# Kernel optimization log

Measured on AMD Instinct MI355X. Metric: run time of the kernel, lower is better.

Reference implementation:

```python
import jax, jax.numpy as jnp
import numpy as np

DIM = 1024
NUM_HEADS = 16
HEAD_DIM = DIM // NUM_HEADS
HIDDEN = 4 * DIM
EPS = 1e-5


def rmsnorm(x, w):
    var = jnp.mean(jnp.square(x), axis=-1, keepdims=True)
    return x * jax.lax.rsqrt(var + EPS) * w


def setup_inputs() -> dict:
    key = jax.random.key(0)
    ks = jax.random.split(key, 10)
    s = 0.02
    return {
        "x": jax.random.normal(ks[0], (2, 2048, DIM), dtype=jnp.float32),
        "wq": jax.random.normal(ks[1], (DIM, DIM), dtype=jnp.float32) * s,
        "wk": jax.random.normal(ks[2], (DIM, DIM), dtype=jnp.float32) * s,
        "wv": jax.random.normal(ks[3], (DIM, DIM), dtype=jnp.float32) * s,
        "wo": jax.random.normal(ks[4], (DIM, DIM), dtype=jnp.float32) * s,
        "wgate": jax.random.normal(ks[5], (HIDDEN, DIM), dtype=jnp.float32) * s,
        "wup": jax.random.normal(ks[6], (HIDDEN, DIM), dtype=jnp.float32) * s,
        "wdown": jax.random.normal(ks[7], (DIM, HIDDEN), dtype=jnp.float32) * s,
        "norm1_w": jnp.ones((DIM,), dtype=jnp.float32),
        "norm2_w": jnp.ones((DIM,), dtype=jnp.float32),
    }


def reference(x, wq, wk, wv, wo, wgate, wup, wdown, norm1_w, norm2_w):
    B, S, _ = x.shape
    residual = x
    h = rmsnorm(x, norm1_w)
    # torch Linear: y = x @ W.T  (W is [out, in])
    q = (h @ wq.T).reshape(B, S, NUM_HEADS, HEAD_DIM)
    k = (h @ wk.T).reshape(B, S, NUM_HEADS, HEAD_DIM)
    v = (h @ wv.T).reshape(B, S, NUM_HEADS, HEAD_DIM)
    scale = HEAD_DIM ** -0.5
    # [B, H, S, S] scores, causal mask
    scores = jnp.einsum("bqhd,bkhd->bhqk", q, k) * scale
    causal = jnp.tril(jnp.ones((S, S), dtype=bool))
    scores = jnp.where(causal, scores, -jnp.inf)
    attn = jax.nn.softmax(scores, axis=-1)
    out = jnp.einsum("bhqk,bkhd->bqhd", attn, v).reshape(B, S, DIM)
    x = residual + out @ wo.T
    residual = x
    h = rmsnorm(x, norm2_w)
    mlp = (jax.nn.silu(h @ wgate.T) * (h @ wup.T)) @ wdown.T
    return residual + mlp
```

## Files before the change

kernel.cpp:

```cpp
#include <hip/hip_runtime.h>
#include <stdint.h>

typedef __attribute__((ext_vector_type(4))) float  f32x4;
typedef __attribute__((ext_vector_type(8))) __bf16 bf16x8;
typedef __attribute__((ext_vector_type(4))) unsigned short us4;

__device__ __forceinline__ unsigned short f2bf(float f) {
  unsigned int u = __float_as_uint(f);
  unsigned int r = (u + 0x7fffu + ((u >> 16) & 1u)) >> 16;
  return (unsigned short)r;
}
__device__ __forceinline__ float bf2f(unsigned short h) {
  return __uint_as_float(((unsigned int)h) << 16);
}
__device__ __forceinline__ void gload16(const void* g, void* l) {
  __builtin_amdgcn_global_load_lds((const __attribute__((address_space(1))) void*)g,
                                   (__attribute__((address_space(3))) void*)l, 16, 0, 0);
}

__global__ __launch_bounds__(256) void convert_w(
    const float* __restrict__ wq, const float* __restrict__ wk, const float* __restrict__ wv,
    const float* __restrict__ wo, const float* __restrict__ wg, const float* __restrict__ wu,
    const float* __restrict__ wd, unsigned short* __restrict__ dst)
{
  long vid = (long)blockIdx.x * 256 + threadIdx.x;
  long e = vid * 4;
  const float* s; long base;
  if (e < (1L << 22)) { int wi = (int)(e >> 20); s = wi == 0 ? wq : wi == 1 ? wk : wi == 2 ? wv : wo; base = (long)wi << 20; }
  else if (e < (2L << 22)) { s = wg; base = 1L << 22; }
  else if (e < (3L << 22)) { s = wu; base = 2L << 22; }
  else                     { s = wd; base = 3L << 22; }
  f32x4 v = *(const f32x4*)(s + (e - base));
  us4 o; o.x = f2bf(v.x); o.y = f2bf(v.y); o.z = f2bf(v.z); o.w = f2bf(v.w);
  *(us4*)(dst + e) = o;
}

__global__ __launch_bounds__(256) void rmsnorm_k(const float* __restrict__ x,
                                                 const float* __restrict__ w,
                                                 unsigned short* __restrict__ h)
{
  const int row = blockIdx.x, t = threadIdx.x;
  const float* xr = x + (long)row * 1024;
  f32x4 v = *(const f32x4*)(xr + t * 4);
  float ss = v.x * v.x + v.y * v.y + v.z * v.z + v.w * v.w;
  #pragma unroll
  for (int o = 32; o > 0; o >>= 1) ss += __shfl_xor(ss, o);
  __shared__ float red[4];
  if ((t & 63) == 0) red[t >> 6] = ss;
  __syncthreads();
  ss = red[0] + red[1] + red[2] + red[3];
  float sc = rsqrtf(ss * (1.0f / 1024.0f) + 1e-5f);
  f32x4 wv = *(const f32x4*)(w + t * 4);
  us4 o4;
  o4.x = f2bf(v.x * sc * wv.x);
  o4.y = f2bf(v.y * sc * wv.y);
  o4.z = f2bf(v.z * sc * wv.z);
  o4.w = f2bf(v.w * sc * wv.w);
  *(us4*)(h + (long)row * 1024 + t * 4) = o4;
}

template<int EPI, int BM>
__global__ __launch_bounds__(256) void gemm_bt(
    const unsigned short* __restrict__ A, const unsigned short* __restrict__ B,
    int M, int N, int K, void* __restrict__ out0,
    const float* __restrict__ resid, const unsigned short* __restrict__ gbuf)
{
  constexpr int MI = (BM == 128) ? 4 : 2;
  __shared__ __align__(16) unsigned short Al[BM * 64];
  __shared__ __align__(16) unsigned short Bl[128 * 64];
  const int t = threadIdx.x;
  const int lane = t & 63;
  const int wid = t >> 6;
  const int wr = wid >> 1, wc = wid & 1;
  const long m0 = (long)blockIdx.x * BM;
  const long n0 = (long)blockIdx.y * 128;
  const int lr = lane & 15, lk = (lane >> 4) * 8;
  f32x4 acc[MI][4] = {};
  const int trow = t >> 3, tcol = (t & 7) * 8;
  const unsigned short* Ag = A + (m0 + trow) * (long)K + tcol;
  const unsigned short* Bg = B + (n0 + trow) * (long)K + tcol;
  unsigned short* Ald = Al + trow * 64 + tcol;
  unsigned short* Bld = Bl + trow * 64 + tcol;
  const int nkt = K >> 6;
  for (int kt = 0; kt < nkt; ++kt) {
    #pragma unroll
    for (int i = 0; i < BM / 32; ++i)
      gload16(Ag + (long)kt * 64 + (long)i * 32 * K, Ald + i * 2048);
    #pragma unroll
    for (int i = 0; i < 4; ++i)
      gload16(Bg + (long)kt * 64 + (long)i * 32 * K, Bld + i * 2048);
    __syncthreads();
    #pragma unroll
    for (int kk = 0; kk < 64; kk += 32) {
      bf16x8 af[MI], bfr[4];
      #pragma unroll
      for (int mi = 0; mi < MI; ++mi)
        af[mi] = *(const bf16x8*)&Al[(wr * (MI * 16) + mi * 16 + lr) * 64 + kk + lk];
      #pragma unroll
      for (int ni = 0; ni < 4; ++ni)
        bfr[ni] = *(const bf16x8*)&Bl[(wc * 64 + ni * 16 + lr) * 64 + kk + lk];
      #pragma unroll
      for (int mi = 0; mi < MI; ++mi)
        #pragma unroll
        for (int ni = 0; ni < 4; ++ni)
          acc[mi][ni] = __builtin_amdgcn_mfma_f32_16x16x32_bf16(af[mi], bfr[ni], acc[mi][ni], 0, 0, 0);
    }
    __syncthreads();
  }
  const int lg = lane >> 4;
  #pragma unroll
  for (int mi = 0; mi < MI; ++mi)
    #pragma unroll
    for (int ni = 0; ni < 4; ++ni)
      #pragma unroll
      for (int j = 0; j < 4; ++j) {
        long row = m0 + wr * (MI * 16) + mi * 16 + lg * 4 + j;
        long col = n0 + wc * 64 + ni * 16 + lr;
        float v = acc[mi][ni][j];
        if (EPI == 0) {
          unsigned short* qkv = (unsigned short*)out0;
          long b = row >> 11, s = row & 2047;
          if (col < 1024) {
            long hh = col >> 6, d = col & 63;
            qkv[((b * 16 + hh) * 2048 + s) * 64 + d] = f2bf(v);
          } else if (col < 2048) {
            long c = col - 1024, hh = c >> 6, d = c & 63;
            qkv[4194304 + ((b * 16 + hh) * 2048 + s) * 64 + d] = f2bf(v);
          } else {
            long c = col - 2048, hh = c >> 6, d = c & 63;
            qkv[8388608 + ((b * 16 + hh) * 64 + d) * 2048 + s] = f2bf(v);
          }
        } else if (EPI == 1) {
          ((float*)out0)[row * N + col] = resid[row * N + col] + v;
        } else if (EPI == 2) {
          ((unsigned short*)out0)[row * N + col] = f2bf(v);
        } else {
          float g = bf2f(gbuf[row * N + col]);
          float sg = g / (1.0f + __expf(-g));
          ((unsigned short*)out0)[row * N + col] = f2bf(sg * v);
        }
      }
}

__global__ __launch_bounds__(256) void attn_k(
    const unsigned short* __restrict__ qb, const unsigned short* __restrict__ kb,
    const unsigned short* __restrict__ vtb, unsigned short* __restrict__ ob)
{
  __shared__ __align__(16) unsigned short Kl[2 * 4096];
  __shared__ __align__(16) unsigned short Vl[2 * 4096];
  __shared__ __align__(16) unsigned short Pl[4 * 1024];
  const int t = threadIdx.x, lane = t & 63, w = t >> 6;
  const int pid = blockIdx.x;
  const int bh = blockIdx.y;
  const int lr = lane & 15, lg = lane >> 4;
  const long kvbase = (long)bh * 2048 * 64;
  const float SC = 0.125f * 1.4426950408889634f;

  const int trow = t >> 3;
  const int csw = (((t & 7) ^ (trow & 7)) * 8);
  auto stage = [&](int buf, int kt2) {
    #pragma unroll
    for (int i = 0; i < 2; ++i) {
      gload16(&kb[kvbase + (long)(kt2 * 64 + i * 32 + trow) * 64 + csw],
              &Kl[buf * 4096 + i * 2048 + t * 8]);
      gload16(&vtb[kvbase + (long)(i * 32 + trow) * 2048 + kt2 * 64 + csw],
              &Vl[buf * 4096 + i * 2048 + t * 8]);
    }
  };
  auto swz = [](const unsigned short* base, int row, int col) -> const bf16x8* {
    int b = ((row << 7) + (col << 1)) ^ ((row & 7) << 4);
    return (const bf16x8*)((const char*)base + b);
  };

  #pragma unroll 1
  for (int pass = 0; pass < 2; ++pass) {
    const int qt = pass ? pid : (31 - pid);
    const int q0 = qt * 64;
    bf16x8 qf[2];
    #pragma unroll
    for (int kk = 0; kk < 2; ++kk)
      qf[kk] = *(const bf16x8*)&qb[kvbase + (long)(q0 + w * 16 + lr) * 64 + kk * 32 + lg * 8];
    f32x4 oacc[4] = {};
    float mi_[4], li_[4];
    #pragma unroll
    for (int j = 0; j < 4; ++j) { mi_[j] = -1e30f; li_[j] = 0.f; }

    stage(0, 0);
    __syncthreads();
    int cur = 0;
    for (int kt = 0; kt <= qt; ++kt) {
      if (kt < qt) stage(cur ^ 1, kt + 1);
      f32x4 sa[4] = {};
      #pragma unroll
      for (int kk = 0; kk < 2; ++kk)
        #pragma unroll
        for (int ni = 0; ni < 4; ++ni) {
          bf16x8 kf = *swz(&Kl[cur * 4096], ni * 16 + lr, kk * 32 + lg * 8);
          sa[ni] = __builtin_amdgcn_mfma_f32_16x16x32_bf16(qf[kk], kf, sa[ni], 0, 0, 0);
        }
      float p[4][4];
      const bool diag = (kt == qt);
      #pragma unroll
      for (int ni = 0; ni < 4; ++ni)
        #pragma unroll
        for (int j = 0; j < 4; ++j) {
          float sv = sa[ni][j] * SC;
          if (diag && (ni * 16 + lr > w * 16 + lg * 4 + j)) sv = -1e30f;
          p[ni][j] = sv;
        }
      float mx4[4];
      #pragma unroll
      for (int j = 0; j < 4; ++j) {
        float mx = fmaxf(fmaxf(p[0][j], p[1][j]), fmaxf(p[2][j], p[3][j]));
        mx = fmaxf(mx, __shfl_xor(mx, 1));
        mx = fmaxf(mx, __shfl_xor(mx, 2));
        mx = fmaxf(mx, __shfl_xor(mx, 4));
        mx = fmaxf(mx, __shfl_xor(mx, 8));
        mx4[j] = mx;
      }
      float g = fmaxf(fmaxf(mx4[0] - mi_[0], mx4[1] - mi_[1]),
                      fmaxf(mx4[2] - mi_[2], mx4[3] - mi_[3]));
      if (!__all(g <= 8.0f)) {
        #pragma unroll
        for (int j = 0; j < 4; ++j) {
          float mnew = fmaxf(mi_[j], mx4[j]);
          float a = exp2f(mi_[j] - mnew);
          mi_[j] = mnew;
          li_[j] *= a;
          #pragma unroll
          for (int f = 0; f < 4; ++f) oacc[f][j] *= a;
        }
      }
      #pragma unroll
      for (int j = 0; j < 4; ++j) {
        float rs = 0.f;
        #pragma unroll
        for (int ni = 0; ni < 4; ++ni) { float e = exp2f(p[ni][j] - mi_[j]); p[ni][j] = e; rs += e; }
        rs += __shfl_xor(rs, 1); rs += __shfl_xor(rs, 2);
        rs += __shfl_xor(rs, 4); rs += __shfl_xor(rs, 8);
        li_[j] += rs;
      }
      unsigned short* pw = &Pl[w * 1024];
      #pragma unroll
      for (int ni = 0; ni < 4; ++ni)
        #pragma unroll
        for (int j = 0; j < 4; ++j) {
          int row = lg * 4 + j, col = ni * 16 + lr;
          int b = ((row << 7) + (col << 1)) ^ ((row & 7) << 4);
          *(unsigned short*)((char*)pw + b) = f2bf(p[ni][j]);
        }
      #pragma unroll
      for (int kk = 0; kk < 2; ++kk) {
        bf16x8 pf = *swz(pw, lr, kk * 32 + lg * 8);
        #pragma unroll
        for (int f = 0; f < 4; ++f) {
          bf16x8 vf = *swz(&Vl[cur * 4096], f * 16 + lr, kk * 32 + lg * 8);
          oacc[f] = __builtin_amdgcn_mfma_f32_16x16x32_bf16(pf, vf, oacc[f], 0, 0, 0);
        }
      }
      __syncthreads();
      cur ^= 1;
    }
    const long b = bh >> 4, hh = bh & 15;
    #pragma unroll
    for (int f = 0; f < 4; ++f)
      #pragma unroll
      for (int j = 0; j < 4; ++j) {
        long s = q0 + w * 16 + lg * 4 + j;
        long c = hh * 64 + f * 16 + lr;
        ob[(b * 2048 + s) * 1024 + c] = f2bf(oacc[f][j] / li_[j]);
      }
  }
}

extern "C" void kernel_launch(void* const* d_in, const int* in_sizes, int n_in,
                              void* d_out, int out_size, void* d_ws, size_t ws_size,
                              hipStream_t stream) {
  const float* x     = (const float*)d_in[0];
  const float* wq    = (const float*)d_in[1];
  const float* wk    = (const float*)d_in[2];
  const float* wv    = (const float*)d_in[3];
  const float* wo    = (const float*)d_in[4];
  const float* wgate = (const float*)d_in[5];
  const float* wup   = (const float*)d_in[6];
  const float* wdown = (const float*)d_in[7];
  const float* n1w   = (const float*)d_in[8];
  const float* n2w   = (const float*)d_in[9];
  float* out = (float*)d_out;

  char* ws = (char*)d_ws;
  unsigned short* wbf   = (unsigned short*)ws;
  unsigned short* h_bf  = (unsigned short*)(ws + (32L << 20));
  unsigned short* qkv   = (unsigned short*)(ws + (40L << 20));
  unsigned short* attno = (unsigned short*)(ws + (64L << 20));
  float*          x2    = (float*)(ws + (72L << 20));
  unsigned short* h2    = (unsigned short*)(ws + (88L << 20));
  unsigned short* gateb = (unsigned short*)(ws + (96L << 20));

  const unsigned short* wq_bf = wbf;
  const unsigned short* wo_bf = wbf + 3L * 1048576;
  const unsigned short* wg_bf = wbf + 4194304L;
  const unsigned short* wu_bf = wbf + 8388608L;
  const unsigned short* wd_bf = wbf + 12582912L;

  convert_w<<<16384, 256, 0, stream>>>(wq, wk, wv, wo, wgate, wup, wdown, wbf);
  rmsnorm_k<<<4096, 256, 0, stream>>>(x, n1w, h_bf);
  gemm_bt<0, 128><<<dim3(32, 24), 256, 0, stream>>>(h_bf, wq_bf, 4096, 3072, 1024, qkv, nullptr, nullptr);
  attn_k<<<dim3(16, 32), 256, 0, stream>>>(qkv, qkv + 4194304, qkv + 8388608, attno);
  gemm_bt<1, 64><<<dim3(64, 8), 256, 0, stream>>>(attno, wo_bf, 4096, 1024, 1024, x2, x, nullptr);
  rmsnorm_k<<<4096, 256, 0, stream>>>(x2, n2w, h2);
  gemm_bt<2, 128><<<dim3(32, 32), 256, 0, stream>>>(h2, wg_bf, 4096, 4096, 1024, gateb, nullptr, nullptr);
  gemm_bt<3, 128><<<dim3(32, 32), 256, 0, stream>>>(h2, wu_bf, 4096, 4096, 1024, gateb, nullptr, gateb);
  gemm_bt<1, 64><<<dim3(64, 8), 256, 0, stream>>>(gateb, wd_bf, 4096, 1024, 4096, out, x2, nullptr);
}
```

Measured before the change: 477.5 us.

## Add 256x256-tile 8-wave GEMM kernel for MLP gate and up projections

Adds a new gemm8 kernel using 512 threads (8 waves) and 256x256 output tiles, with double-buffered LDS staging via direct global-to-LDS loads, XOR swizzling, grid remapping for L2 locality, and setprio around the MFMA blocks. The gate and up GEMMs now use it instead of the 128-tile gemm_bt. The aim is more data reuse per LDS load and better overlap of prefetch with MFMA. The cost is heavy register pressure from 32 accumulator fragments and only 256 workgroups, which may leave some CUs idle.

```diff
diff --git a/kernel.cpp b/kernel.cpp
--- a/kernel.cpp
+++ b/kernel.cpp
@@ -132,12 +132,107 @@
           }
         } else if (EPI == 1) {
           ((float*)out0)[row * N + col] = resid[row * N + col] + v;
-        } else if (EPI == 2) {
-          ((unsigned short*)out0)[row * N + col] = f2bf(v);
+        }
+      }
+}
+
+template<int EPI>
+__global__ __launch_bounds__(512, 2) void gemm8(
+    const unsigned short* __restrict__ A, const unsigned short* __restrict__ B,
+    int M, int N, int K, unsigned short* __restrict__ out0,
+    const unsigned short* __restrict__ gbuf)
+{
+  __shared__ __align__(16) unsigned short Asl[2][2][8192];
+  __shared__ __align__(16) unsigned short Bsl[2][2][8192];
+  const int t = threadIdx.x;
+  const int lane = t & 63, w = t >> 6;
+  const int wr = w >> 2, wc = w & 3;
+  const int lr = lane & 15, lg = lane >> 4;
+  const int nwg = gridDim.x * gridDim.y;
+  int lid = blockIdx.y * gridDim.x + blockIdx.x;
+  if ((nwg & 7) == 0) lid = (lid & 7) * (nwg >> 3) + (lid >> 3);
+  const long m0 = (long)(lid % gridDim.x) * 256;
+  const long n0 = (long)(lid / gridDim.x) * 256;
+
+  const int swb = ((lr >> 2) & 1) << 5;
+  const int colx0 = (lg * 16) ^ swb;
+  const int colx1 = (64 + lg * 16) ^ swb;
+
+  const int scol = ((t & 7) * 8) ^ (((t >> 5) & 1) << 4);
+  const int srow = t >> 3;
+
+  auto stage = [&](int kt, int buf) {
+    const long kc = (long)kt * 64 + scol;
+    #pragma unroll
+    for (int h = 0; h < 2; ++h)
+      #pragma unroll
+      for (int j = 0; j < 2; ++j) {
+        const int row = h * 128 + j * 64 + srow;
+        gload16(&A[(m0 + row) * (long)K + kc], &Asl[buf][h][j * 4096 + t * 8]);
+        gload16(&B[(n0 + row) * (long)K + kc], &Bsl[buf][h][j * 4096 + t * 8]);
+      }
+  };
+
+  f32x4 acc[8][4] = {};
+  const int nkt = K >> 6;
+
+  stage(0, 0);
+  __syncthreads();
+
+  for (int kt = 0; kt < nkt; ++kt) {
+    const int p = kt & 1;
+    const char* Ab = (const char*)Asl[p][wr];
+    const char* Bb = (const char*)Bsl[p][wc >> 1];
+    bf16x8 breg[4][2];
+    #pragma unroll
+    for (int ni = 0; ni < 4; ++ni) {
+      const int brow = (wc & 1) * 64 + ni * 16 + lr;
+      breg[ni][0] = *(const bf16x8*)(Bb + brow * 128 + colx0);
+      breg[ni][1] = *(const bf16x8*)(Bb + brow * 128 + colx1);
+    }
+    #pragma unroll
+    for (int q2 = 0; q2 < 4; ++q2) {
+      bf16x8 areg[2][2];
+      #pragma unroll
+      for (int mi = 0; mi < 2; ++mi) {
+        const int arow = q2 * 32 + mi * 16 + lr;
+        areg[mi][0] = *(const bf16x8*)(Ab + arow * 128 + colx0);
+        areg[mi][1] = *(const bf16x8*)(Ab + arow * 128 + colx1);
+      }
+      if (q2 == 0 && kt + 1 < nkt) stage(kt + 1, p ^ 1);
+      __builtin_amdgcn_s_setprio(1);
+      #pragma unroll
+      for (int mi = 0; mi < 2; ++mi)
+        #pragma unroll
+        for (int ni = 0; ni < 4; ++ni) {
+          acc[q2 * 2 + mi][ni] = __builtin_amdgcn_mfma_f32_16x16x32_bf16(
+              areg[mi][0], breg[ni][0], acc[q2 * 2 + mi][ni], 0, 0, 0);
+          acc[q2 * 2 + mi][ni] = __builtin_amdgcn_mfma_f32_16x16x32_bf16(
+              areg[mi][1], breg[ni][1], acc[q2 * 2 + mi][ni], 0, 0, 0);
+        }
+      __builtin_amdgcn_s_setprio(0);
+      if (q2 < 3) __builtin_amdgcn_s_barrier();
+    }
+    asm volatile("s_waitcnt vmcnt(0)" ::: "memory");
+    __builtin_amdgcn_s_barrier();
+    __builtin_amdgcn_sched_barrier(0);
+  }
+
+  #pragma unroll
+  for (int fi = 0; fi < 8; ++fi)
+    #pragma unroll
+    for (int ni = 0; ni < 4; ++ni)
+      #pragma unroll
+      for (int j = 0; j < 4; ++j) {
+        long row = m0 + wr * 128 + fi * 16 + lg * 4 + j;
+        long col = n0 + wc * 64 + ni * 16 + lr;
+        float v = acc[fi][ni][j];
+        if (EPI == 2) {
+          out0[row * N + col] = f2bf(v);
         } else {
           float g = bf2f(gbuf[row * N + col]);
           float sg = g / (1.0f + __expf(-g));
-          ((unsigned short*)out0)[row * N + col] = f2bf(sg * v);
+          out0[row * N + col] = f2bf(sg * v);
         }
       }
 }
@@ -309,7 +404,7 @@
   attn_k<<<dim3(16, 32), 256, 0, stream>>>(qkv, qkv + 4194304, qkv + 8388608, attno);
   gemm_bt<1, 64><<<dim3(64, 8), 256, 0, stream>>>(attno, wo_bf, 4096, 1024, 1024, x2, x, nullptr);
   rmsnorm_k<<<4096, 256, 0, stream>>>(x2, n2w, h2);
-  gemm_bt<2, 128><<<dim3(32, 32), 256, 0, stream>>>(h2, wg_bf, 4096, 4096, 1024, gateb, nullptr, nullptr);
-  gemm_bt<3, 128><<<dim3(32, 32), 256, 0, stream>>>(h2, wu_bf, 4096, 4096, 1024, gateb, nullptr, gateb);
+  gemm8<2><<<dim3(16, 16), 512, 0, stream>>>(h2, wg_bf, 4096, 4096, 1024, gateb, nullptr);
+  gemm8<3><<<dim3(16, 16), 512, 0, stream>>>(h2, wu_bf, 4096, 4096, 1024, gateb, gateb);
   gemm_bt<1, 64><<<dim3(64, 8), 256, 0, stream>>>(gateb, wd_bf, 4096, 1024, 4096, out, x2, nullptr);
 }
```

New measurement: 448.6 us. -6.1%, faster.
